# Kernel optimization log

Measured on AMD Instinct MI355X. Metric: run time of the kernel, lower is better.

The kernel has to match this reference:

```python
import jax, jax.numpy as jnp
import numpy as np

B, D, H, S = 32768, 512, 8, 3  # batch, stream_dim, heads, num_streams
DH = D // H
EPS = 1e-5


def setup_inputs() -> dict:
    key = jax.random.key(0)
    ks = jax.random.split(key, 16)
    sc = lambda fan_in: 1.0 / np.sqrt(fan_in)
    return {
        "kinematic_h": jax.random.normal(ks[0], (B, D), jnp.float32),
        "color_h": jax.random.normal(ks[1], (B, D), jnp.float32),
        "spinor_h": jax.random.normal(ks[2], (B, D), jnp.float32),
        # MultiheadAttention packed in-proj and out-proj
        "w_in": jax.random.normal(ks[3], (3 * D, D), jnp.float32) * sc(D),
        "b_in": jnp.zeros((3 * D,), jnp.float32),
        "w_out": jax.random.normal(ks[4], (D, D), jnp.float32) * sc(D),
        "b_out": jnp.zeros((D,), jnp.float32),
        # stream gate: Linear(3D -> 3) + softmax
        "w_gate": jax.random.normal(ks[5], (S, S * D), jnp.float32) * sc(S * D),
        "b_gate": jnp.zeros((S,), jnp.float32),
        # fusion MLP: Linear(3D -> 2D), SiLU, Linear(2D -> D)
        "w1": jax.random.normal(ks[6], (2 * D, S * D), jnp.float32) * sc(S * D),
        "b1": jnp.zeros((2 * D,), jnp.float32),
        "w2": jax.random.normal(ks[7], (D, 2 * D), jnp.float32) * sc(2 * D),
        "b2": jnp.zeros((D,), jnp.float32),
        # LayerNorm
        "gamma": jnp.ones((D,), jnp.float32),
        "beta": jnp.zeros((D,), jnp.float32),
    }


def reference(kinematic_h, color_h, spinor_h, w_in, b_in, w_out, b_out,
              w_gate, b_gate, w1, b1, w2, b2, gamma, beta):
    stacked = jnp.stack([kinematic_h, color_h, spinor_h], axis=1)  # [B,S,D]
    b = stacked.shape[0]
    # self-attention (Q=K=V=stacked), packed QKV projection
    qkv = stacked @ w_in.T + b_in  # [B,S,3D]
    q, k, v = jnp.split(qkv, 3, axis=-1)
    q = q.reshape(b, S, H, DH)
    k = k.reshape(b, S, H, DH)
    v = v.reshape(b, S, H, DH)
    scores = jnp.einsum("bqhd,bkhd->bhqk", q, k) / np.sqrt(DH)
    attn = jax.nn.softmax(scores, axis=-1)
    out = jnp.einsum("bhqk,bkhd->bqhd", attn, v).reshape(b, S, D)
    attn_out = stacked + (out @ w_out.T + b_out)  # residual, [B,S,D]
    # gating softmax over streams
    flat = attn_out.reshape(b, S * D)
    gates = jax.nn.softmax(flat @ w_gate.T + b_gate, axis=-1)[..., None]  # [B,S,1]
    gated = (attn_out * gates).reshape(b, S * D)
    # fusion MLP (dropout=eval no-op)
    h = jax.nn.silu(gated @ w1.T + b1)
    fused = h @ w2.T + b2  # [B,D]
    # LayerNorm
    mu = jnp.mean(fused, axis=-1, keepdims=True)
    var = jnp.var(fused, axis=-1, keepdims=True)
    return (fused - mu) * jax.lax.rsqrt(var + EPS) * gamma + beta
```

## Files before the change

### kernel.cpp

```cpp
#include <hip/hip_runtime.h>
#include <hip/hip_bf16.h>
#include <stdint.h>


typedef float f32x4 __attribute__((ext_vector_type(4)));
typedef short bf16x8 __attribute__((ext_vector_type(8)));

__device__ __forceinline__ float bf2f(unsigned short h) {
  return __uint_as_float(((unsigned)h) << 16);
}
__device__ __forceinline__ unsigned short f2bf(float f) {
  __hip_bfloat16 h = __float2bfloat16(f);
  return *reinterpret_cast<unsigned short*>(&h);
}
__device__ __forceinline__ unsigned pack2bf(float lo, float hi) {
  __hip_bfloat162 h2 = __float22bfloat162_rn(make_float2(lo, hi));
  return *reinterpret_cast<unsigned*>(&h2);
}
__device__ __forceinline__ uint2 f2bf4p(float4 v) {
  return make_uint2(pack2bf(v.x, v.y), pack2bf(v.z, v.w));
}

__device__ __forceinline__ void async_cp16(const void* g, void* lds) {
  __builtin_amdgcn_global_load_lds(
      (const __attribute__((address_space(1))) void*)g,
      (__attribute__((address_space(3))) void*)lds, 16, 0, 0);
}

__global__ void __launch_bounds__(256) cvtall(const float4* __restrict__ w_in,
                                              const float4* __restrict__ w_out,
                                              const float4* __restrict__ w1,
                                              const float4* __restrict__ w2,
                                              uint2* __restrict__ dst) {
  int i = blockIdx.x * 256 + threadIdx.x;
  const float4* s;
  int off;
  if (i < 196608)      { s = w_in;  off = 0; }
  else if (i < 262144) { s = w_out; off = 196608; }
  else if (i < 655360) { s = w1;    off = 262144; }
  else                 { s = w2;    off = 655360; }
  dst[i] = f2bf4p(s[i - off]);
}

__global__ void __launch_bounds__(256)
qkv_attn(const float* __restrict__ X0,
         const float* __restrict__ X1,
         const float* __restrict__ X2,
         const unsigned short* __restrict__ Wi,
         const float* __restrict__ bin,
         unsigned short* __restrict__ Sout,
         unsigned short* __restrict__ AO) {
  __shared__ unsigned short lds[96 * 200];
  unsigned short* Abuf = lds;
  unsigned short* Bbuf = lds + 6144;

  const int t = threadIdx.x;
  const int lane = t & 63;
  const int wave = t >> 6;
  const int wm = wave >> 1, wn = wave & 1;

  const int ny = gridDim.y;
  const int id = blockIdx.y * 8 + blockIdx.x;
  const int xcd = id & 7, j = id >> 3;
  const int h = j & 7;
  const long m0 = (long)(xcd * (ny >> 3) + (j >> 3)) * 96;

  const int trow = t >> 3;
  const int swz = ((t & 7) ^ (trow & 7)) << 3;
  const long b0 = m0 / 3;
  const float* Aptr[3];
  unsigned short* Sptr[3];
#pragma unroll
  for (int r = 0; r < 3; r++) {
    const int rl = trow + 32 * r;
    const int br = rl / 3;
    const int sr = rl - 3 * br;
    const float* X = (sr == 0) ? X0 : (sr == 1) ? X1 : X2;
    Aptr[r] = X + (b0 + br) * 512 + swz;
    Sptr[r] = Sout + (m0 + rl) * 512 + swz;
  }
  const unsigned short* Bg = Wi + ((long)h * 64 + trow) * 512 + swz;
  unsigned short* AsD = Abuf + t * 8;
  unsigned short* BsD = Bbuf + t * 8;

  f32x4 acc[3][6] = {};
  const int arow0 = wm * 48 + (lane & 15);
  const int brow0 = wn * 96 + (lane & 15);

  float4 Alo[3], Ahi[3];
#pragma unroll
  for (int r = 0; r < 3; r++) {
    Alo[r] = *(const float4*)(Aptr[r]);
    Ahi[r] = *(const float4*)(Aptr[r] + 4);
  }

  for (int k0 = 0; k0 < 512; k0 += 64) {
    __syncthreads();
    const bool sw = ((k0 >> 6) == h);
#pragma unroll
    for (int r = 0; r < 3; r++) {
      const uint4 uv = make_uint4(
          pack2bf(Alo[r].x, Alo[r].y), pack2bf(Alo[r].z, Alo[r].w),
          pack2bf(Ahi[r].x, Ahi[r].y), pack2bf(Ahi[r].z, Ahi[r].w));
      *(uint4*)(AsD + r * 2048) = uv;
      if (sw) *(uint4*)(Sptr[r] + k0) = uv;
    }
#pragma unroll
    for (int r = 0; r < 6; r++)
      async_cp16(Bg + (long)((r >> 1) * 512 + (r & 1) * 32) * 512 + k0, BsD + r * 2048);
    __syncthreads();
    if (k0 + 64 < 512) {
#pragma unroll
      for (int r = 0; r < 3; r++) {
        Alo[r] = *(const float4*)(Aptr[r] + k0 + 64);
        Ahi[r] = *(const float4*)(Aptr[r] + k0 + 68);
      }
    }
#pragma unroll
    for (int kk = 0; kk < 2; kk++) {
      const int sc = ((kk * 4 + (lane >> 4)) ^ (lane & 7)) << 3;
      bf16x8 af[3], bfr[6];
#pragma unroll
      for (int mt = 0; mt < 3; mt++)
        af[mt] = *(const bf16x8*)&Abuf[(arow0 + mt * 16) * 64 + sc];
#pragma unroll
      for (int nt = 0; nt < 6; nt++)
        bfr[nt] = *(const bf16x8*)&Bbuf[(brow0 + nt * 16) * 64 + sc];
#pragma unroll
      for (int mt = 0; mt < 3; mt++)
#pragma unroll
        for (int nt = 0; nt < 6; nt++)
          acc[mt][nt] = __builtin_amdgcn_mfma_f32_16x16x32_bf16(
              af[mt], bfr[nt], acc[mt][nt], 0, 0, 0);
    }
  }

  __syncthreads();
  const int crow0 = wm * 48 + ((lane >> 4) << 2);
  const int ccol0 = wn * 96 + (lane & 15);
#pragma unroll
  for (int nt = 0; nt < 6; nt++) {
    const int col = ccol0 + nt * 16;
    const float bv = bin[(col >> 6) * 512 + h * 64 + (col & 63)];
#pragma unroll
    for (int mt = 0; mt < 3; mt++) {
      const int rb = (crow0 + mt * 16) * 200 + col;
      const unsigned p01 = pack2bf(acc[mt][nt][0] + bv, acc[mt][nt][1] + bv);
      const unsigned p23 = pack2bf(acc[mt][nt][2] + bv, acc[mt][nt][3] + bv);
      lds[rb]       = (unsigned short)p01;
      lds[rb + 200] = (unsigned short)(p01 >> 16);
      lds[rb + 400] = (unsigned short)p23;
      lds[rb + 600] = (unsigned short)(p23 >> 16);
    }
  }
  __syncthreads();

  const int bi = lane >> 3;
  const int l8 = lane & 7;
  const int r0 = (wave * 8 + bi) * 3;
  float q[3][8], k[3][8], v[3][8];
#pragma unroll
  for (int s = 0; s < 3; s++) {
    const unsigned short* rowp = &lds[(r0 + s) * 200 + l8 * 8];
    uint4 qu = *(const uint4*)(rowp);
    uint4 ku = *(const uint4*)(rowp + 64);
    uint4 vu = *(const uint4*)(rowp + 128);
    const unsigned* qw = (const unsigned*)&qu;
    const unsigned* kw = (const unsigned*)&ku;
    const unsigned* vw = (const unsigned*)&vu;
#pragma unroll
    for (int jj = 0; jj < 4; jj++) {
      q[s][2 * jj]     = __uint_as_float(qw[jj] << 16);
      q[s][2 * jj + 1] = __uint_as_float(qw[jj] & 0xffff0000u);
      k[s][2 * jj]     = __uint_as_float(kw[jj] << 16);
      k[s][2 * jj + 1] = __uint_as_float(kw[jj] & 0xffff0000u);
      v[s][2 * jj]     = __uint_as_float(vw[jj] << 16);
      v[s][2 * jj + 1] = __uint_as_float(vw[jj] & 0xffff0000u);
    }
  }
  float p[3][3];
#pragma unroll
  for (int s = 0; s < 3; s++)
#pragma unroll
    for (int u = 0; u < 3; u++) {
      float d = 0.f;
#pragma unroll
      for (int e = 0; e < 8; e++) d = fmaf(q[s][e], k[u][e], d);
      p[s][u] = d;
    }
#pragma unroll
  for (int m = 1; m < 8; m <<= 1)
#pragma unroll
    for (int s = 0; s < 3; s++)
#pragma unroll
      for (int u = 0; u < 3; u++) p[s][u] += __shfl_xor(p[s][u], m, 64);

  unsigned short* ob = AO + (m0 + r0) * 512 + h * 64 + l8 * 8;
#pragma unroll
  for (int s = 0; s < 3; s++) {
    float a0 = p[s][0] * 0.125f, a1 = p[s][1] * 0.125f, a2 = p[s][2] * 0.125f;
    float mx = fmaxf(a0, fmaxf(a1, a2));
    float e0 = __expf(a0 - mx), e1 = __expf(a1 - mx), e2 = __expf(a2 - mx);
    float inv = 1.0f / (e0 + e1 + e2);
    unsigned ow[4];
#pragma unroll
    for (int jj = 0; jj < 4; jj++) {
      float lo = (e0 * v[0][2 * jj] + e1 * v[1][2 * jj] + e2 * v[2][2 * jj]) * inv;
      float hi = (e0 * v[0][2 * jj + 1] + e1 * v[1][2 * jj + 1] + e2 * v[2][2 * jj + 1]) * inv;
      ow[jj] = pack2bf(lo, hi);
    }
    *(uint4*)(ob + s * 512) = *(uint4*)ow;
  }
}

enum { EPI_BF16 = 0, EPI_RES = 1, EPI_SILU = 2, EPI_F32 = 3 };

template <int EPI>
__global__ void __launch_bounds__(256)
gemm_bt(const unsigned short* __restrict__ A,
        const unsigned short* __restrict__ W,
        const float* __restrict__ bias,
        const unsigned short* __restrict__ Res,
        void* __restrict__ Out,
        int K, int N) {
  __shared__ unsigned short As[128 * 64];
  __shared__ unsigned short Bs[128 * 64];
  const int t = threadIdx.x;
  const int lane = t & 63;
  const int wave = t >> 6;
  const int wm = wave >> 1, wn = wave & 1;

  const int nb = gridDim.x;
  const int nblocks = nb * gridDim.y;
  const int id = blockIdx.y * nb + blockIdx.x;
  const int lid = ((nblocks & 7) == 0) ? ((id & 7) * (nblocks >> 3) + (id >> 3)) : id;
  const long bm = (long)(lid / nb) * 128;
  const long bn = (long)(lid % nb) * 128;

  const int srow = t >> 3;
  const int schunk = ((t & 7) ^ (srow & 7)) << 3;
  const unsigned short* Ag = A + (bm + srow) * (long)K + schunk;
  const unsigned short* Wg = W + (bn + srow) * (long)K + schunk;
  unsigned short* AsD = As + t * 8;
  unsigned short* BsD = Bs + t * 8;

  f32x4 acc[4][4] = {};
  const int arow0 = wm * 64 + (lane & 15);
  const int brow0 = wn * 64 + (lane & 15);

  for (int k0 = 0; k0 < K; k0 += 64) {
    __syncthreads();
#pragma unroll
    for (int i = 0; i < 4; i++) {
      async_cp16(Ag + (long)(i * 32) * K + k0, AsD + i * 2048);
      async_cp16(Wg + (long)(i * 32) * K + k0, BsD + i * 2048);
    }
    __syncthreads();
#pragma unroll
    for (int kk = 0; kk < 2; kk++) {
      const int sc = ((kk * 4 + (lane >> 4)) ^ (lane & 7)) << 3;
      bf16x8 af[4], bfr[4];
#pragma unroll
      for (int mt = 0; mt < 4; mt++)
        af[mt] = *(const bf16x8*)&As[(arow0 + mt * 16) * 64 + sc];
#pragma unroll
      for (int nt = 0; nt < 4; nt++)
        bfr[nt] = *(const bf16x8*)&Bs[(brow0 + nt * 16) * 64 + sc];
#pragma unroll
      for (int mt = 0; mt < 4; mt++)
#pragma unroll
        for (int nt = 0; nt < 4; nt++)
          acc[mt][nt] = __builtin_amdgcn_mfma_f32_16x16x32_bf16(
              af[mt], bfr[nt], acc[mt][nt], 0, 0, 0);
    }
  }

  const long row0 = bm + wm * 64 + ((lane >> 4) << 2);
  const int col0 = (int)bn + wn * 64 + (lane & 15);
#pragma unroll
  for (int nt = 0; nt < 4; nt++) {
    const int col = col0 + nt * 16;
    const float bv = bias[col];
#pragma unroll
    for (int mt = 0; mt < 4; mt++) {
      const long rbase = row0 + mt * 16;
#pragma unroll
      for (int r = 0; r < 4; r++) {
        float v = acc[mt][nt][r] + bv;
        const long idx = (rbase + r) * (long)N + col;
        if (EPI == EPI_RES) v += bf2f(Res[idx]);
        if (EPI == EPI_SILU) v = v * (1.0f / (1.0f + __expf(-v)));
        if (EPI == EPI_F32)
          ((float*)Out)[idx] = v;
        else
          ((unsigned short*)Out)[idx] = f2bf(v);
      }
    }
  }
}

__global__ void __launch_bounds__(512)
gemm_silu256(const unsigned short* __restrict__ A,
             const unsigned short* __restrict__ W,
             const float* __restrict__ bias,
             unsigned short* __restrict__ Out) {
  constexpr int K = 1536, N = 1024, NT = 24;
  constexpr int NSH = 8192, NDB = 16384;
  __shared__ unsigned short As[2 * NDB];
  __shared__ unsigned short Bs[2 * NDB];
  const int t = threadIdx.x;
  const int lane = t & 63;
  const int wave = t >> 6;
  const int wm = wave >> 2, wn = wave & 3;
  const int l15 = lane & 15, lg = lane >> 4;

  const int nb = gridDim.x;
  const int nblocks = nb * gridDim.y;
  const int id = blockIdx.y * nb + blockIdx.x;
  const int lid = (id & 7) * (nblocks >> 3) + (id >> 3);
  const long bm = (long)(lid / nb) * 256;
  const long bn = (long)(lid % nb) * 256;

  const int r0s = t >> 2, pc = t & 3;
  const int c0 = pc ^ ((r0s >> 1) & 3);
  const int r1s = r0s + 128;
  const int c1 = pc ^ ((r1s >> 1) & 3);
  const unsigned short* Ag0 = A + (bm + r0s) * (long)K + c0 * 8;
  const unsigned short* Ag1 = A + (bm + r1s) * (long)K + c1 * 8;
  const unsigned short* Wg0 = W + (bn + r0s) * (long)K + c0 * 8;
  const unsigned short* Wg1 = W + (bn + r1s) * (long)K + c1 * 8;

#define STA(d, kh, kb) do { \
    async_cp16(Ag0 + (kb), &As[(d) * NDB + (kh) * NSH + t * 8]); \
    async_cp16(Ag1 + (kb), &As[(d) * NDB + (kh) * NSH + 4096 + t * 8]); } while (0)
#define STB(d, kh, kb) do { \
    async_cp16(Wg0 + (kb), &Bs[(d) * NDB + (kh) * NSH + t * 8]); \
    async_cp16(Wg1 + (kb), &Bs[(d) * NDB + (kh) * NSH + 4096 + t * 8]); } while (0)

  const int ach = (lg ^ ((l15 >> 1) & 3)) << 3;
  const int aoff = (wm * 128 + l15) * 32 + ach;
  const int boff = (wn * 64 + l15) * 32 + ach;

  f32x4 acc[8][4] = {};

  STA(0, 0, 0);  STB(0, 0, 0);
  STA(0, 1, 32); STB(0, 1, 32);
  STA(1, 0, 64); STB(1, 0, 64);
  asm volatile("s_waitcnt vmcnt(8)" ::: "memory");
  __builtin_amdgcn_s_barrier();

  for (int tt = 0; tt < NT; ++tt) {
    const int d = tt & 1, dn = d ^ 1;
    const bool s1 = (tt + 1 < NT), s2 = (tt + 2 < NT);
    const int kb1 = (tt + 1) * 64, kb2 = (tt + 2) * 64;
    const unsigned short* Ab = &As[d * NDB];
    const unsigned short* Bb = &Bs[d * NDB];
    bf16x8 af[4], bfr[4];

#pragma unroll
    for (int i = 0; i < 4; ++i) af[i] = *(const bf16x8*)&Ab[aoff + i * 512];
#pragma unroll
    for (int i = 0; i < 4; ++i) bfr[i] = *(const bf16x8*)&Bb[boff + i * 512];
    if (s1) STA(dn, 1, kb1 + 32);
    __builtin_amdgcn_s_barrier();
    asm volatile("s_waitcnt lgkmcnt(0)" ::: "memory");
    __builtin_amdgcn_s_setprio(1);
#pragma unroll
    for (int mi = 0; mi < 4; ++mi)
#pragma unroll
      for (int ni = 0; ni < 4; ++ni)
        acc[mi][ni] = __builtin_amdgcn_mfma_f32_16x16x32_bf16(
            af[mi], bfr[ni], acc[mi][ni], 0, 0, 0);
    __builtin_amdgcn_s_setprio(0);
    __builtin_amdgcn_s_barrier();

#pragma unroll
    for (int i = 0; i < 4; ++i) af[i] = *(const bf16x8*)&Ab[aoff + (4 + i) * 512];
    if (s1) STB(dn, 1, kb1 + 32);
    __builtin_amdgcn_s_barrier();
    asm volatile("s_waitcnt lgkmcnt(0)" ::: "memory");
    __builtin_amdgcn_s_setprio(1);
#pragma unroll
    for (int mi = 0; mi < 4; ++mi)
#pragma unroll
      for (int ni = 0; ni < 4; ++ni)
        acc[4 + mi][ni] = __builtin_amdgcn_mfma_f32_16x16x32_bf16(
            af[mi], bfr[ni], acc[4 + mi][ni], 0, 0, 0);
    __builtin_amdgcn_s_setprio(0);
    asm volatile("s_waitcnt vmcnt(8)" ::: "memory");
    __builtin_amdgcn_s_barrier();

#pragma unroll
    for (int i = 0; i < 4; ++i) af[i] = *(const bf16x8*)&Ab[NSH + aoff + i * 512];
#pragma unroll
    for (int i = 0; i < 4; ++i) bfr[i] = *(const bf16x8*)&Bb[NSH + boff + i * 512];
    if (s2) STA(d, 0, kb2);
    __builtin_amdgcn_s_barrier();
    asm volatile("s_waitcnt lgkmcnt(0)" ::: "memory");
    __builtin_amdgcn_s_setprio(1);
#pragma unroll
    for (int mi = 0; mi < 4; ++mi)
#pragma unroll
      for (int ni = 0; ni < 4; ++ni)
        acc[mi][ni] = __builtin_amdgcn_mfma_f32_16x16x32_bf16(
            af[mi], bfr[ni], acc[mi][ni], 0, 0, 0);
    __builtin_amdgcn_s_setprio(0);
    __builtin_amdgcn_s_barrier();

#pragma unroll
    for (int i = 0; i < 4; ++i) af[i] = *(const bf16x8*)&Ab[NSH + aoff + (4 + i) * 512];
    if (s2) STB(d, 0, kb2);
    __builtin_amdgcn_s_barrier();
    asm volatile("s_waitcnt lgkmcnt(0)" ::: "memory");
    __builtin_amdgcn_s_setprio(1);
#pragma unroll
    for (int mi = 0; mi < 4; ++mi)
#pragma unroll
      for (int ni = 0; ni < 4; ++ni)
        acc[4 + mi][ni] = __builtin_amdgcn_mfma_f32_16x16x32_bf16(
            af[mi], bfr[ni], acc[4 + mi][ni], 0, 0, 0);
    __builtin_amdgcn_s_setprio(0);
    asm volatile("s_waitcnt vmcnt(8)" ::: "memory");
    __builtin_amdgcn_s_barrier();
  }
#undef STA
#undef STB

  const long grow0 = bm + wm * 128 + (lg << 2);
  const int col0 = (int)bn + wn * 64 + l15;
#pragma unroll
  for (int nt = 0; nt < 4; ++nt) {
    const int col = col0 + nt * 16;
    const float bv = bias[col];
#pragma unroll
    for (int mt = 0; mt < 8; ++mt) {
      const long rb = grow0 + mt * 16;
#pragma unroll
      for (int r = 0; r < 4; ++r) {
        float v = acc[mt][nt][r] + bv;
        v = v * (1.0f / (1.0f + __expf(-v)));
        Out[(rb + r) * (long)N + col] = f2bf(v);
      }
    }
  }
}

__global__ void __launch_bounds__(512)
gemm_ln(const unsigned short* __restrict__ A,
        const unsigned short* __restrict__ W,
        const float* __restrict__ bias,
        const float* __restrict__ gamma,
        const float* __restrict__ beta,
        float* __restrict__ Out,
        int K) {
  __shared__ unsigned short As[64 * 64];
  __shared__ unsigned short Bs[512 * 64];
  __shared__ float stats[8][64][2];
  const int t = threadIdx.x;
  const int lane = t & 63;
  const int wave = t >> 6;

  const int nblocks = gridDim.x;
  const int id = blockIdx.x;
  const int lid = ((nblocks & 7) == 0) ? ((id & 7) * (nblocks >> 3) + (id >> 3)) : id;
  const long bm = (long)lid * 64;

  const int srow = t >> 3;
  const int sch = ((t & 7) ^ (srow & 7)) << 3;
  const unsigned short* Ag = A + (bm + srow) * (long)K + sch;
  const unsigned short* Wg = W + (long)srow * K + sch;
  unsigned short* AsD = As + t * 8;
  unsigned short* BsD = Bs + t * 8;

  f32x4 acc[4][4] = {};
  const int arow0 = lane & 15;
  const int brow0 = wave * 64 + (lane & 15);

  for (int k0 = 0; k0 < K; k0 += 64) {
    __syncthreads();
    async_cp16(Ag + k0, AsD);
#pragma unroll
    for (int i = 0; i < 8; i++)
      async_cp16(Wg + (long)(i * 64) * K + k0, BsD + i * 4096);
    __syncthreads();
#pragma unroll
    for (int kk = 0; kk < 2; kk++) {
      const int sc = ((kk * 4 + (lane >> 4)) ^ (lane & 7)) << 3;
      bf16x8 af[4], bfr[4];
#pragma unroll
      for (int mt = 0; mt < 4; mt++)
        af[mt] = *(const bf16x8*)&As[(arow0 + mt * 16) * 64 + sc];
#pragma unroll
      for (int nt = 0; nt < 4; nt++)
        bfr[nt] = *(const bf16x8*)&Bs[(brow0 + nt * 16) * 64 + sc];
#pragma unroll
      for (int mt = 0; mt < 4; mt++)
#pragma unroll
        for (int nt = 0; nt < 4; nt++)
          acc[mt][nt] = __builtin_amdgcn_mfma_f32_16x16x32_bf16(
              af[mt], bfr[nt], acc[mt][nt], 0, 0, 0);
    }
  }

  const int colb = wave * 64 + (lane & 15);
  float bv[4], gm[4], be[4];
#pragma unroll
  for (int nt = 0; nt < 4; nt++) {
    bv[nt] = bias[colb + nt * 16];
    gm[nt] = gamma[colb + nt * 16];
    be[nt] = beta[colb + nt * 16];
  }
#pragma unroll
  for (int mt = 0; mt < 4; mt++)
#pragma unroll
    for (int r = 0; r < 4; r++) {
      float s = 0.f, ss = 0.f;
#pragma unroll
      for (int nt = 0; nt < 4; nt++) {
        const float v = acc[mt][nt][r] + bv[nt];
        s += v; ss += v * v;
      }
#pragma unroll
      for (int m = 1; m < 16; m <<= 1) {
        s += __shfl_xor(s, m, 64);
        ss += __shfl_xor(ss, m, 64);
      }
      if ((lane & 15) == 0) {
        const int rl = mt * 16 + ((lane >> 4) << 2) + r;
        stats[wave][rl][0] = s;
        stats[wave][rl][1] = ss;
      }
    }
  __syncthreads();
#pragma unroll
  for (int mt = 0; mt < 4; mt++)
#pragma unroll
    for (int r = 0; r < 4; r++) {
      const int rl = mt * 16 + ((lane >> 4) << 2) + r;
      float s = 0.f, ss = 0.f;
#pragma unroll
      for (int w = 0; w < 8; w++) {
        s += stats[w][rl][0];
        ss += stats[w][rl][1];
      }
      const float mean = s * (1.0f / 512.0f);
      const float var = ss * (1.0f / 512.0f) - mean * mean;
      const float rstd = rsqrtf(var + 1e-5f);
      float* orow = Out + (bm + rl) * 512;
#pragma unroll
      for (int nt = 0; nt < 4; nt++) {
        const float v = acc[mt][nt][r] + bv[nt];
        orow[colb + nt * 16] = (v - mean) * rstd * gm[nt] + be[nt];
      }
    }
}

__global__ void __launch_bounds__(256) gate3(const unsigned short* AT,
                                             const float* __restrict__ WG,
                                             const float* __restrict__ BG,
                                             unsigned short* G) {
  int row = blockIdx.x * 4 + (threadIdx.x >> 6);
  int lane = threadIdx.x & 63;
  const unsigned short* rp = AT + (long)row * 1536 + lane * 8;
  float x[3][8];
  float p[3] = {0.f, 0.f, 0.f};
#pragma unroll
  for (int seg = 0; seg < 3; seg++) {
    uint4 u = *(const uint4*)(rp + seg * 512);
    const unsigned* uw = (const unsigned*)&u;
#pragma unroll
    for (int j = 0; j < 4; j++) {
      x[seg][2 * j]     = __uint_as_float(uw[j] << 16);
      x[seg][2 * j + 1] = __uint_as_float(uw[j] & 0xffff0000u);
    }
    const int e0 = seg * 512 + lane * 8;
#pragma unroll
    for (int g = 0; g < 3; g++) {
      const float* wp = WG + g * 1536 + e0;
#pragma unroll
      for (int e = 0; e < 8; e++) p[g] = fmaf(x[seg][e], wp[e], p[g]);
    }
  }
#pragma unroll
  for (int m = 1; m < 64; m <<= 1)
#pragma unroll
    for (int g = 0; g < 3; g++) p[g] += __shfl_xor(p[g], m, 64);
  float g0 = p[0] + BG[0], g1 = p[1] + BG[1], g2 = p[2] + BG[2];
  float mx = fmaxf(g0, fmaxf(g1, g2));
  g0 = __expf(g0 - mx); g1 = __expf(g1 - mx); g2 = __expf(g2 - mx);
  float inv = 1.0f / (g0 + g1 + g2);
  float gs[3] = {g0 * inv, g1 * inv, g2 * inv};
  unsigned short* op = G + (long)row * 1536 + lane * 8;
#pragma unroll
  for (int seg = 0; seg < 3; seg++) {
    unsigned ow[4];
#pragma unroll
    for (int j = 0; j < 4; j++)
      ow[j] = pack2bf(x[seg][2 * j] * gs[seg], x[seg][2 * j + 1] * gs[seg]);
    *(uint4*)(op + seg * 512) = *(uint4*)ow;
  }
}

extern "C" void kernel_launch(void* const* d_in, const int* in_sizes, int n_in,
                              void* d_out, int out_size, void* d_ws, size_t ws_size,
                              hipStream_t stream) {
  const float* kin    = (const float*)d_in[0];
  const float* colr   = (const float*)d_in[1];
  const float* spi    = (const float*)d_in[2];
  const float* w_in   = (const float*)d_in[3];
  const float* b_in   = (const float*)d_in[4];
  const float* w_out  = (const float*)d_in[5];
  const float* b_out  = (const float*)d_in[6];
  const float* w_gate = (const float*)d_in[7];
  const float* b_gate = (const float*)d_in[8];
  const float* w1     = (const float*)d_in[9];
  const float* b1     = (const float*)d_in[10];
  const float* w2     = (const float*)d_in[11];
  const float* b2     = (const float*)d_in[12];
  const float* gamma  = (const float*)d_in[13];
  const float* beta   = (const float*)d_in[14];
  float* out = (float*)d_out;

  long Bc = 32768;
  while (Bc > 1024 && (size_t)(6291456 + 9216 * Bc) > ws_size) Bc >>= 1;
  const int nch = (int)(32768 / Bc);

  char* ws = (char*)d_ws;
  unsigned short* Wic = (unsigned short*)(ws);
  unsigned short* Woc = (unsigned short*)(ws + 1572864);
  unsigned short* W1c = (unsigned short*)(ws + 2097152);
  unsigned short* W2c = (unsigned short*)(ws + 5242880);
  char* Sb  = ws + 6291456;
  char* AOb = Sb + 3072 * Bc;
  char* ATb = AOb + 3072 * Bc;

  cvtall<<<3072, 256, 0, stream>>>((const float4*)w_in, (const float4*)w_out,
                                   (const float4*)w1, (const float4*)w2,
                                   (uint2*)ws);

  for (int c = 0; c < nch; c++) {
    const long boff = (long)c * Bc;
    unsigned short* S_c  = (unsigned short*)Sb;
    unsigned short* AO_c = (unsigned short*)AOb;
    unsigned short* AT_c = (unsigned short*)ATb;
    unsigned short* G_c  = AT_c;
    unsigned short* H_c  = (unsigned short*)AOb;

    qkv_attn<<<dim3(8, (int)(Bc / 32)), 256, 0, stream>>>(
        kin + boff * 512, colr + boff * 512, spi + boff * 512,
        Wic, b_in, S_c, AO_c);
    gemm_bt<EPI_RES><<<dim3(4, (int)(3 * Bc / 128)), 256, 0, stream>>>(
        AO_c, Woc, b_out, S_c, AT_c, 512, 512);
    gate3<<<(int)(Bc / 4), 256, 0, stream>>>(AT_c, w_gate, b_gate, G_c);
    gemm_silu256<<<dim3(4, (int)(Bc / 256)), 512, 0, stream>>>(
        G_c, W1c, b1, H_c);
    gemm_ln<<<(int)(Bc / 64), 512, 0, stream>>>(
        H_c, W2c, b2, gamma, beta, out + boff * 512, 1024);
  }
}
```

Baseline: 746.1 us.

## Replace out-projection GEMM with 256x256 double-buffered pipelined residual kernel

Swaps the generic 128x128 single-buffered gemm_bt used for the attention out-projection plus residual for a specialised 256x256-tile, 512-thread kernel. The new kernel is modelled on the existing gemm_silu256. It double-buffers LDS, issues async global-to-LDS copies interleaved with MFMA phases, and uses s_setprio around the MFMA blocks. The aim is to hide load latency behind compute and raise data reuse per tile, at the cost of a larger LDS footprint and fewer blocks in the grid.

```diff
diff --git a/kernel.cpp b/kernel.cpp
--- a/kernel.cpp
+++ b/kernel.cpp
@@ -210,92 +210,6 @@
       ow[jj] = pack2bf(lo, hi);
     }
     *(uint4*)(ob + s * 512) = *(uint4*)ow;
-  }
-}
-
-enum { EPI_BF16 = 0, EPI_RES = 1, EPI_SILU = 2, EPI_F32 = 3 };
-
-template <int EPI>
-__global__ void __launch_bounds__(256)
-gemm_bt(const unsigned short* __restrict__ A,
-        const unsigned short* __restrict__ W,
-        const float* __restrict__ bias,
-        const unsigned short* __restrict__ Res,
-        void* __restrict__ Out,
-        int K, int N) {
-  __shared__ unsigned short As[128 * 64];
-  __shared__ unsigned short Bs[128 * 64];
-  const int t = threadIdx.x;
-  const int lane = t & 63;
-  const int wave = t >> 6;
-  const int wm = wave >> 1, wn = wave & 1;
-
-  const int nb = gridDim.x;
-  const int nblocks = nb * gridDim.y;
-  const int id = blockIdx.y * nb + blockIdx.x;
-  const int lid = ((nblocks & 7) == 0) ? ((id & 7) * (nblocks >> 3) + (id >> 3)) : id;
-  const long bm = (long)(lid / nb) * 128;
-  const long bn = (long)(lid % nb) * 128;
-
-  const int srow = t >> 3;
-  const int schunk = ((t & 7) ^ (srow & 7)) << 3;
-  const unsigned short* Ag = A + (bm + srow) * (long)K + schunk;
-  const unsigned short* Wg = W + (bn + srow) * (long)K + schunk;
-  unsigned short* AsD = As + t * 8;
-  unsigned short* BsD = Bs + t * 8;
-
-  f32x4 acc[4][4] = {};
-  const int arow0 = wm * 64 + (lane & 15);
-  const int brow0 = wn * 64 + (lane & 15);
-
-  for (int k0 = 0; k0 < K; k0 += 64) {
-    __syncthreads();
-#pragma unroll
-    for (int i = 0; i < 4; i++) {
-      async_cp16(Ag + (long)(i * 32) * K + k0, AsD + i * 2048);
-      async_cp16(Wg + (long)(i * 32) * K + k0, BsD + i * 2048);
-    }
-    __syncthreads();
-#pragma unroll
-    for (int kk = 0; kk < 2; kk++) {
-      const int sc = ((kk * 4 + (lane >> 4)) ^ (lane & 7)) << 3;
-      bf16x8 af[4], bfr[4];
-#pragma unroll
-      for (int mt = 0; mt < 4; mt++)
-        af[mt] = *(const bf16x8*)&As[(arow0 + mt * 16) * 64 + sc];
-#pragma unroll
-      for (int nt = 0; nt < 4; nt++)
-        bfr[nt] = *(const bf16x8*)&Bs[(brow0 + nt * 16) * 64 + sc];
-#pragma unroll
-      for (int mt = 0; mt < 4; mt++)
-#pragma unroll
-        for (int nt = 0; nt < 4; nt++)
-          acc[mt][nt] = __builtin_amdgcn_mfma_f32_16x16x32_bf16(
-              af[mt], bfr[nt], acc[mt][nt], 0, 0, 0);
-    }
-  }
-
-  const long row0 = bm + wm * 64 + ((lane >> 4) << 2);
-  const int col0 = (int)bn + wn * 64 + (lane & 15);
-#pragma unroll
-  for (int nt = 0; nt < 4; nt++) {
-    const int col = col0 + nt * 16;
-    const float bv = bias[col];
-#pragma unroll
-    for (int mt = 0; mt < 4; mt++) {
-      const long rbase = row0 + mt * 16;
-#pragma unroll
-      for (int r = 0; r < 4; r++) {
-        float v = acc[mt][nt][r] + bv;
-        const long idx = (rbase + r) * (long)N + col;
-        if (EPI == EPI_RES) v += bf2f(Res[idx]);
-        if (EPI == EPI_SILU) v = v * (1.0f / (1.0f + __expf(-v)));
-        if (EPI == EPI_F32)
-          ((float*)Out)[idx] = v;
-        else
-          ((unsigned short*)Out)[idx] = f2bf(v);
-      }
-    }
   }
 }
 
@@ -440,6 +354,153 @@
         float v = acc[mt][nt][r] + bv;
         v = v * (1.0f / (1.0f + __expf(-v)));
         Out[(rb + r) * (long)N + col] = f2bf(v);
+      }
+    }
+  }
+}
+
+__global__ void __launch_bounds__(512)
+gemm_res256(const unsigned short* __restrict__ A,
+            const unsigned short* __restrict__ W,
+            const float* __restrict__ bias,
+            const unsigned short* __restrict__ Res,
+            unsigned short* __restrict__ Out) {
+  constexpr int K = 512, N = 512, NT = 8;
+  constexpr int NSH = 8192, NDB = 16384;
+  __shared__ unsigned short As[2 * NDB];
+  __shared__ unsigned short Bs[2 * NDB];
+  const int t = threadIdx.x;
+  const int lane = t & 63;
+  const int wave = t >> 6;
+  const int wm = wave >> 2, wn = wave & 3;
+  const int l15 = lane & 15, lg = lane >> 4;
+
+  const int nb = gridDim.x;
+  const int nblocks = nb * gridDim.y;
+  const int id = blockIdx.y * nb + blockIdx.x;
+  const int lid = (id & 7) * (nblocks >> 3) + (id >> 3);
+  const long bm = (long)(lid / nb) * 256;
+  const long bn = (long)(lid % nb) * 256;
+
+  const int r0s = t >> 2, pc = t & 3;
+  const int c0 = pc ^ ((r0s >> 1) & 3);
+  const int r1s = r0s + 128;
+  const int c1 = pc ^ ((r1s >> 1) & 3);
+  const unsigned short* Ag0 = A + (bm + r0s) * (long)K + c0 * 8;
+  const unsigned short* Ag1 = A + (bm + r1s) * (long)K + c1 * 8;
+  const unsigned short* Wg0 = W + (bn + r0s) * (long)K + c0 * 8;
+  const unsigned short* Wg1 = W + (bn + r1s) * (long)K + c1 * 8;
+
+#define STA(d, kh, kb) do { \
+    async_cp16(Ag0 + (kb), &As[(d) * NDB + (kh) * NSH + t * 8]); \
+    async_cp16(Ag1 + (kb), &As[(d) * NDB + (kh) * NSH + 4096 + t * 8]); } while (0)
+#define STB(d, kh, kb) do { \
+    async_cp16(Wg0 + (kb), &Bs[(d) * NDB + (kh) * NSH + t * 8]); \
+    async_cp16(Wg1 + (kb), &Bs[(d) * NDB + (kh) * NSH + 4096 + t * 8]); } while (0)
+
+  const int ach = (lg ^ ((l15 >> 1) & 3)) << 3;
+  const int aoff = (wm * 128 + l15) * 32 + ach;
+  const int boff = (wn * 64 + l15) * 32 + ach;
+
+  f32x4 acc[8][4] = {};
+
+  STA(0, 0, 0);  STB(0, 0, 0);
+  STA(0, 1, 32); STB(0, 1, 32);
+  STA(1, 0, 64); STB(1, 0, 64);
+  asm volatile("s_waitcnt vmcnt(8)" ::: "memory");
+  __builtin_amdgcn_s_barrier();
+
+  for (int tt = 0; tt < NT; ++tt) {
+    const int d = tt & 1, dn = d ^ 1;
+    const bool s1 = (tt + 1 < NT), s2 = (tt + 2 < NT);
+    const int kb1 = (tt + 1) * 64, kb2 = (tt + 2) * 64;
+    const unsigned short* Ab = &As[d * NDB];
+    const unsigned short* Bb = &Bs[d * NDB];
+    bf16x8 af[4], bfr[4];
+
+#pragma unroll
+    for (int i = 0; i < 4; ++i) af[i] = *(const bf16x8*)&Ab[aoff + i * 512];
+#pragma unroll
+    for (int i = 0; i < 4; ++i) bfr[i] = *(const bf16x8*)&Bb[boff + i * 512];
+    if (s1) STA(dn, 1, kb1 + 32);
+    __builtin_amdgcn_s_barrier();
+    asm volatile("s_waitcnt lgkmcnt(0)" ::: "memory");
+    __builtin_amdgcn_s_setprio(1);
+#pragma unroll
+    for (int mi = 0; mi < 4; ++mi)
+#pragma unroll
+      for (int ni = 0; ni < 4; ++ni)
+        acc[mi][ni] = __builtin_amdgcn_mfma_f32_16x16x32_bf16(
+            af[mi], bfr[ni], acc[mi][ni], 0, 0, 0);
+    __builtin_amdgcn_s_setprio(0);
+    __builtin_amdgcn_s_barrier();
+
+#pragma unroll
+    for (int i = 0; i < 4; ++i) af[i] = *(const bf16x8*)&Ab[aoff + (4 + i) * 512];
+    if (s1) STB(dn, 1, kb1 + 32);
+    __builtin_amdgcn_s_barrier();
+    asm volatile("s_waitcnt lgkmcnt(0)" ::: "memory");
+    __builtin_amdgcn_s_setprio(1);
+#pragma unroll
+    for (int mi = 0; mi < 4; ++mi)
+#pragma unroll
+      for (int ni = 0; ni < 4; ++ni)
+        acc[4 + mi][ni] = __builtin_amdgcn_mfma_f32_16x16x32_bf16(
+            af[mi], bfr[ni], acc[4 + mi][ni], 0, 0, 0);
+    __builtin_amdgcn_s_setprio(0);
+    asm volatile("s_waitcnt vmcnt(8)" ::: "memory");
+    __builtin_amdgcn_s_barrier();
+
+#pragma unroll
+    for (int i = 0; i < 4; ++i) af[i] = *(const bf16x8*)&Ab[NSH + aoff + i * 512];
+#pragma unroll
+    for (int i = 0; i < 4; ++i) bfr[i] = *(const bf16x8*)&Bb[NSH + boff + i * 512];
+    if (s2) STA(d, 0, kb2);
+    __builtin_amdgcn_s_barrier();
+    asm volatile("s_waitcnt lgkmcnt(0)" ::: "memory");
+    __builtin_amdgcn_s_setprio(1);
+#pragma unroll
+    for (int mi = 0; mi < 4; ++mi)
+#pragma unroll
+      for (int ni = 0; ni < 4; ++ni)
+        acc[mi][ni] = __builtin_amdgcn_mfma_f32_16x16x32_bf16(
+            af[mi], bfr[ni], acc[mi][ni], 0, 0, 0);
+    __builtin_amdgcn_s_setprio(0);
+    __builtin_amdgcn_s_barrier();
+
+#pragma unroll
+    for (int i = 0; i < 4; ++i) af[i] = *(const bf16x8*)&Ab[NSH + aoff + (4 + i) * 512];
+    if (s2) STB(d, 0, kb2);
+    __builtin_amdgcn_s_barrier();
+    asm volatile("s_waitcnt lgkmcnt(0)" ::: "memory");
+    __builtin_amdgcn_s_setprio(1);
+#pragma unroll
+    for (int mi = 0; mi < 4; ++mi)
+#pragma unroll
+      for (int ni = 0; ni < 4; ++ni)
+        acc[4 + mi][ni] = __builtin_amdgcn_mfma_f32_16x16x32_bf16(
+            af[mi], bfr[ni], acc[4 + mi][ni], 0, 0, 0);
+    __builtin_amdgcn_s_setprio(0);
+    asm volatile("s_waitcnt vmcnt(8)" ::: "memory");
+    __builtin_amdgcn_s_barrier();
+  }
+#undef STA
+#undef STB
+
+  const long grow0 = bm + wm * 128 + (lg << 2);
+  const int col0 = (int)bn + wn * 64 + l15;
+#pragma unroll
+  for (int nt = 0; nt < 4; ++nt) {
+    const int col = col0 + nt * 16;
+    const float bv = bias[col];
+#pragma unroll
+    for (int mt = 0; mt < 8; ++mt) {
+      const long rb = grow0 + mt * 16;
+#pragma unroll
+      for (int r = 0; r < 4; ++r) {
+        const long idx = (rb + r) * (long)N + col;
+        float v = acc[mt][nt][r] + bv + bf2f(Res[idx]);
+        Out[idx] = f2bf(v);
       }
     }
   }
@@ -649,8 +710,8 @@
     qkv_attn<<<dim3(8, (int)(Bc / 32)), 256, 0, stream>>>(
         kin + boff * 512, colr + boff * 512, spi + boff * 512,
         Wic, b_in, S_c, AO_c);
-    gemm_bt<EPI_RES><<<dim3(4, (int)(3 * Bc / 128)), 256, 0, stream>>>(
-        AO_c, Woc, b_out, S_c, AT_c, 512, 512);
+    gemm_res256<<<dim3(2, (int)(3 * Bc / 256)), 512, 0, stream>>>(
+        AO_c, Woc, b_out, S_c, AT_c);
     gate3<<<(int)(Bc / 4), 256, 0, stream>>>(AT_c, w_gate, b_gate, G_c);
     gemm_silu256<<<dim3(4, (int)(Bc / 256)), 512, 0, stream>>>(
         G_c, W1c, b1, H_c);
```

After: 808.8 us. 8.4% more time.
